# Optimization experiments

Hardware: AMD Instinct MI355X
Metric: run time of the kernel (lower is better)

Reference implementation:

```python
import jax, jax.numpy as jnp
import numpy as np

B, C, H, W = 4, 64, 64, 64
CI = C // 2  # inter_channels


def setup_inputs() -> dict:
    key = jax.random.key(0)
    k1, k2, k3, k4, k5 = jax.random.split(key, 5)
    x = jax.random.normal(k1, (B, C, H, W), dtype=jnp.float32)
    # 1x1 conv g: in C -> CI (weight [CI, C], bias [CI])
    Wg = jax.random.normal(k2, (CI, C), dtype=jnp.float32) * (1.0 / np.sqrt(C))
    bg = jax.random.normal(k3, (CI,), dtype=jnp.float32) * 0.01
    # 1x1 conv W_z: CI -> C
    Wz = jax.random.normal(k4, (C, CI), dtype=jnp.float32) * (1.0 / np.sqrt(CI))
    bz = jax.random.normal(k5, (C,), dtype=jnp.float32) * 0.01
    return {"x": x, "Wg": Wg, "bg": bg, "Wz": Wz, "bz": bz}


def reference(x, Wg, bg, Wz, bz):
    b, c, h, w = x.shape
    n = h * w
    xf = x.reshape(b, c, n)                       # [B,C,N]
    # g projection (1x1 conv) then flatten: [B,N,CI]
    g_x = jnp.einsum('bcn,oc->bno', xf, Wg) + bg  # [B,N,CI]
    # theta = phi = raw x flattened
    theta = xf.transpose(0, 2, 1)                 # [B,N,C]
    f = jnp.einsum('bnc,bcm->bnm', theta, xf)     # [B,N,N]
    f_div_C = jax.nn.softmax(f, axis=-1)
    y = jnp.einsum('bnm,bmo->bno', f_div_C, g_x)  # [B,N,CI]
    y = y.transpose(0, 2, 1).reshape(b, CI, h, w)  # [B,CI,H,W]
    # W_z projection (1x1 conv) + residual
    W_y = jnp.einsum('oi,bihw->bohw', Wz, y) + bz[None, :, None, None]
    return W_y + x
```

## Files before the change

kernel.cpp:

```cpp
#include <hip/hip_runtime.h>
#include <hip/hip_bf16.h>
#include <math.h>

#define B_  4
#define C_  64
#define N_  4096
#define CI_ 32

typedef __attribute__((ext_vector_type(8))) unsigned short u16x8;
typedef __attribute__((ext_vector_type(8))) __bf16        bf16x8;
typedef __attribute__((ext_vector_type(4))) float         f32x4;

__device__ __forceinline__ unsigned short f2bf(float f) {
    union { float f; unsigned int i; } v; v.f = f;
    unsigned int r = v.i + 0x7FFFu + ((v.i >> 16) & 1u);
    return (unsigned short)(r >> 16);
}

__global__ __launch_bounds__(256) void k_prep(
    const float* __restrict__ x, const float* __restrict__ Wg,
    const float* __restrict__ bg, unsigned short* __restrict__ xT,
    unsigned short* __restrict__ gx, float* __restrict__ diag)
{
    __shared__ __align__(16) float tile[64][68];
    __shared__ float part[4][64][33];
    const int t  = threadIdx.x;
    const int b  = blockIdx.x >> 6;
    const int n0 = (blockIdx.x & 63) * 64;

    #pragma unroll
    for (int pass = 0; pass < 4; ++pass) {
        int c   = (t >> 4) + pass * 16;
        int nl4 = (t & 15) * 4;
        float4 v = *(const float4*)(x + (size_t)(b * C_ + c) * N_ + n0 + nl4);
        *(float4*)&tile[c][nl4] = v;
    }
    __syncthreads();

    {
        const int n  = t >> 2;
        const int cc = (t & 3) * 16;
        u16x8 a, b2;
        #pragma unroll
        for (int j = 0; j < 8; ++j) a[j]  = f2bf(tile[cc + j][n]);
        #pragma unroll
        for (int j = 0; j < 8; ++j) b2[j] = f2bf(tile[cc + 8 + j][n]);
        unsigned short* dst = xT + (size_t)(b * N_ + n0 + n) * C_ + cc;
        *(u16x8*)dst       = a;
        *(u16x8*)(dst + 8) = b2;
    }
    {
        const int nl = t & 63, cq = t >> 6;
        float acc[CI_];
        #pragma unroll
        for (int o = 0; o < CI_; ++o) acc[o] = 0.f;
        float dd = 0.f;
        #pragma unroll 4
        for (int cl = 0; cl < 16; ++cl) {
            int c = cq * 16 + cl;
            float xv = tile[c][nl];
            dd += xv * xv;
            #pragma unroll
            for (int o = 0; o < CI_; ++o) acc[o] += Wg[o * C_ + c] * xv;
        }
        #pragma unroll
        for (int o = 0; o < CI_; ++o) part[cq][nl][o] = acc[o];
        part[cq][nl][32] = dd;
    }
    __syncthreads();
    {
        const int o = t >> 3, nr = (t & 7) * 8;
        u16x8 w;
        #pragma unroll
        for (int j = 0; j < 8; ++j) {
            int n = nr + j;
            float s = part[0][n][o] + part[1][n][o] + part[2][n][o] + part[3][n][o]
                    + bg[o];
            w[j] = f2bf(s);
        }
        *(u16x8*)(gx + (size_t)(b * CI_ + o) * N_ + n0 + nr) = w;
    }
    if (t < 64)
        diag[(size_t)b * N_ + n0 + t] =
            part[0][t][32] + part[1][t][32] + part[2][t][32] + part[3][t][32];
}

__device__ __forceinline__ f32x4 mfma16(bf16x8 a, bf16x8 b, f32x4 c) {
    return __builtin_amdgcn_mfma_f32_16x16x32_bf16(a, b, c, 0, 0, 0);
}

__global__ __launch_bounds__(256, 4) void k_flash(
    const unsigned short* __restrict__ xT, const unsigned short* __restrict__ gx,
    const float* __restrict__ diag,
    float* __restrict__ ypart, float* __restrict__ lpart)
{
    __shared__ __align__(16) char smem[24576];
    unsigned short* xk = (unsigned short*)smem;
    unsigned short* vt = (unsigned short*)(smem + 9216);
    unsigned short* Pl = (unsigned short*)(smem + 14336);

    const int tid  = threadIdx.x;
    const int wave = tid >> 6, lane = tid & 63;
    const int quad = lane >> 4, li = lane & 15;
    const int g = wave >> 1, qh = wave & 1;
    const int bi  = blockIdx.x;
    const int kq  = bi & 3;
    const int qtb = (bi >> 2) & 63;
    const int b   = bi >> 8;
    const int qw  = qtb * 64 + qh * 32;
    const int u   = tid & 127;

    float Kq[2];
    #pragma unroll
    for (int qt = 0; qt < 2; ++qt)
        Kq[qt] = diag[(size_t)b * N_ + qw + qt * 16 + li];

    bf16x8 Qf[2][2];
    #pragma unroll
    for (int qt = 0; qt < 2; ++qt)
        #pragma unroll
        for (int kc = 0; kc < 2; ++kc)
            Qf[qt][kc] = *(const bf16x8*)(xT + (size_t)(b * N_ + qw + qt * 16 + li) * C_
                                          + kc * 32 + quad * 8);

    f32x4 Yf[2][2];
    #pragma unroll
    for (int qt = 0; qt < 2; ++qt)
        #pragma unroll
        for (int ot = 0; ot < 2; ++ot)
            Yf[qt][ot] = (f32x4){0.f, 0.f, 0.f, 0.f};
    float lacc[2] = {0.f, 0.f};

    const int keybase = kq * 1024 + g * 512;

    for (int tl = 0; tl < 16; ++tl) {
        const int k0 = keybase + tl * 32;
        __syncthreads();
        #pragma unroll
        for (int j = 0; j < 2; ++j) {
            int cc2 = u * 2 + j;
            int key = cc2 >> 3, coff = (cc2 & 7) * 8;
            *(u16x8*)(xk + (g * 32 + key) * 72 + coff) =
                *(const u16x8*)(xT + (size_t)(b * N_ + k0 + key) * C_ + coff);
        }
        {
            int o = u >> 2, koff = (u & 3) * 8;
            *(u16x8*)(vt + (g * 32 + o) * 40 + koff) =
                *(const u16x8*)(gx + (size_t)(b * CI_ + o) * N_ + k0 + koff);
        }
        __syncthreads();

        bf16x8 A[2][2];
        #pragma unroll
        for (int kt = 0; kt < 2; ++kt)
            #pragma unroll
            for (int kc = 0; kc < 2; ++kc)
                A[kt][kc] = *(const bf16x8*)(xk + (g * 32 + kt * 16 + li) * 72
                                             + kc * 32 + quad * 8);
        f32x4 S[2][2];
        #pragma unroll
        for (int kt = 0; kt < 2; ++kt)
            #pragma unroll
            for (int qt = 0; qt < 2; ++qt) {
                f32x4 z = (f32x4){0.f, 0.f, 0.f, 0.f};
                z = mfma16(A[kt][0], Qf[qt][0], z);
                S[kt][qt] = mfma16(A[kt][1], Qf[qt][1], z);
            }

        #pragma unroll
        for (int qt = 0; qt < 2; ++qt) {
            float p[2][4];
            #pragma unroll
            for (int kt = 0; kt < 2; ++kt)
                #pragma unroll
                for (int r = 0; r < 4; ++r) {
                    p[kt][r] = __expf(S[kt][qt][r] - Kq[qt]);
                    lacc[qt] += p[kt][r];
                }
            #pragma unroll
            for (int kt = 0; kt < 2; ++kt) {
                uint2 wv;
                wv.x = (unsigned)f2bf(p[kt][0]) | ((unsigned)f2bf(p[kt][1]) << 16);
                wv.y = (unsigned)f2bf(p[kt][2]) | ((unsigned)f2bf(p[kt][3]) << 16);
                *(uint2*)(Pl + (wave * 32 + qt * 16 + li) * 40 + kt * 16 + quad * 4) = wv;
            }
        }

        bf16x8 Ap[2], Bv[2];
        #pragma unroll
        for (int qt = 0; qt < 2; ++qt)
            Ap[qt] = *(const bf16x8*)(Pl + (wave * 32 + qt * 16 + li) * 40 + quad * 8);
        #pragma unroll
        for (int ot = 0; ot < 2; ++ot)
            Bv[ot] = *(const bf16x8*)(vt + (g * 32 + ot * 16 + li) * 40 + quad * 8);
        #pragma unroll
        for (int qt = 0; qt < 2; ++qt)
            #pragma unroll
            for (int ot = 0; ot < 2; ++ot)
                Yf[qt][ot] = mfma16(Ap[qt], Bv[ot], Yf[qt][ot]);
    }

    #pragma unroll
    for (int qt = 0; qt < 2; ++qt) {
        lacc[qt] += __shfl_xor(lacc[qt], 16, 64);
        lacc[qt] += __shfl_xor(lacc[qt], 32, 64);
    }

    __syncthreads();
    float* ym = (float*)smem;

    #pragma unroll
    for (int qt = 0; qt < 2; ++qt) {
        #pragma unroll
        for (int ot = 0; ot < 2; ++ot)
            #pragma unroll
            for (int r = 0; r < 4; ++r)
                ym[(wave * 32 + qt * 16 + quad * 4 + r) * 34 + ot * 16 + li] = Yf[qt][ot][r];
        if (quad == 0)
            ym[(wave * 32 + qt * 16 + li) * 34 + 32] = lacc[qt];
    }
    __syncthreads();
    {
        const int q = tid >> 2, og = tid & 3;
        const int qh2 = q >> 5, ql = q & 31;
        const int w0 = qh2, w1 = 2 + qh2;
        const size_t pbase = (size_t)(b * 64 + qtb) * 4 + kq;
        float* yp = ypart + pbase * 2048 + q * 32;
        #pragma unroll
        for (int j = 0; j < 8; ++j) {
            int o = og * 8 + j;
            yp[o] = ym[(w0 * 32 + ql) * 34 + o] + ym[(w1 * 32 + ql) * 34 + o];
        }
        if (og == 0)
            lpart[pbase * 64 + q] = ym[(w0 * 32 + ql) * 34 + 32]
                                  + ym[(w1 * 32 + ql) * 34 + 32];
    }
}

__global__ __launch_bounds__(256) void k_merge(
    const float* __restrict__ ypart, const float* __restrict__ lpart,
    const float* __restrict__ x, const float* __restrict__ Wz,
    const float* __restrict__ bz, float* __restrict__ out)
{
    __shared__ float yfin[64][33];
    const int t   = threadIdx.x;
    const int b   = blockIdx.x >> 6;
    const int qtb = blockIdx.x & 63;
    const int q0  = qtb * 64;

    {
        const int q = t >> 2, og = t & 3;
        const size_t pb = (size_t)(b * 64 + qtb) * 4;
        float l = lpart[(pb + 0) * 64 + q] + lpart[(pb + 1) * 64 + q]
                + lpart[(pb + 2) * 64 + q] + lpart[(pb + 3) * 64 + q];
        float inv = 1.f / l;
        #pragma unroll
        for (int j = 0; j < 8; ++j) {
            int o = og * 8 + j;
            float acc = 0.f;
            #pragma unroll
            for (int kq = 0; kq < 4; ++kq)
                acc += ypart[(pb + kq) * 2048 + q * 32 + o];
            yfin[q][o] = acc * inv;
        }
    }
    __syncthreads();
    {
        const int q = t & 63, c0 = t >> 6;
        #pragma unroll
        for (int i = 0; i < 16; ++i) {
            int cout = c0 + i * 4;
            float acc = bz[cout];
            #pragma unroll
            for (int o = 0; o < CI_; ++o)
                acc += Wz[cout * CI_ + o] * yfin[q][o];
            size_t oidx = (size_t)(b * C_ + cout) * N_ + q0 + q;
            out[oidx] = acc + x[oidx];
        }
    }
}

extern "C" void kernel_launch(void* const* d_in, const int* in_sizes, int n_in,
                              void* d_out, int out_size, void* d_ws, size_t ws_size,
                              hipStream_t stream) {
    (void)in_sizes; (void)n_in; (void)out_size; (void)ws_size;
    const float* x  = (const float*)d_in[0];
    const float* Wg = (const float*)d_in[1];
    const float* bg = (const float*)d_in[2];
    const float* Wz = (const float*)d_in[3];
    const float* bz = (const float*)d_in[4];
    float* out = (float*)d_out;

    unsigned short* xT = (unsigned short*)d_ws;
    unsigned short* gx = (unsigned short*)((char*)d_ws + 2097152);
    float* diag  = (float*)((char*)d_ws + 3145728);
    float* ypart = (float*)((char*)d_ws + 3211264);
    float* lpart = (float*)((char*)d_ws + 11599872);

    hipLaunchKernelGGL(k_prep,  dim3(B_ * (N_ / 64)),    dim3(256), 0, stream, x, Wg, bg, xT, gx, diag);
    hipLaunchKernelGGL(k_flash, dim3(B_ * 64 * 4),       dim3(256), 0, stream, xT, gx, diag, ypart, lpart);
    hipLaunchKernelGGL(k_merge, dim3(B_ * 64),           dim3(256), 0, stream, ypart, lpart, x, Wz, bz, out);
}
```

Baseline: 115.0 us.

## Load K/V MFMA fragments directly from global memory, drop LDS staging and barriers

Removes the shared-memory staging of key and value tiles, and the two block-wide barriers per iteration, by loading MFMA operands straight from global memory (relying on L1/L2 caching). It also folds the softmax shift into the MFMA accumulator initialisation and uses native bf16 conversion instead of manual rounding. LDS use shrinks, which may raise occupancy. The cost is that each wave does its own uncoalesced global loads with no block-level reuse, and the P tile stays in LDS with no barrier between the per-wave write and read.

```diff
diff --git a/kernel.cpp b/kernel.cpp
--- a/kernel.cpp
+++ b/kernel.cpp
@@ -9,6 +9,7 @@
 
 typedef __attribute__((ext_vector_type(8))) unsigned short u16x8;
 typedef __attribute__((ext_vector_type(8))) __bf16        bf16x8;
+typedef __attribute__((ext_vector_type(4))) __bf16        bf16x4;
 typedef __attribute__((ext_vector_type(4))) float         f32x4;
 
 __device__ __forceinline__ unsigned short f2bf(float f) {
@@ -94,10 +95,8 @@
     const float* __restrict__ diag,
     float* __restrict__ ypart, float* __restrict__ lpart)
 {
-    __shared__ __align__(16) char smem[24576];
-    unsigned short* xk = (unsigned short*)smem;
-    unsigned short* vt = (unsigned short*)(smem + 9216);
-    unsigned short* Pl = (unsigned short*)(smem + 14336);
+    __shared__ __align__(16) char smem[17408];
+    unsigned short* Pl = (unsigned short*)smem;
 
     const int tid  = threadIdx.x;
     const int wave = tid >> 6, lane = tid & 63;
@@ -108,19 +107,21 @@
     const int qtb = (bi >> 2) & 63;
     const int b   = bi >> 8;
     const int qw  = qtb * 64 + qh * 32;
-    const int u   = tid & 127;
-
-    float Kq[2];
+
+    const unsigned short* xb = xT + (size_t)b * N_ * C_;
+    const unsigned short* gb = gx + (size_t)b * CI_ * N_;
+
+    float nKq[2];
     #pragma unroll
     for (int qt = 0; qt < 2; ++qt)
-        Kq[qt] = diag[(size_t)b * N_ + qw + qt * 16 + li];
+        nKq[qt] = -diag[(size_t)b * N_ + qw + qt * 16 + li];
 
     bf16x8 Qf[2][2];
     #pragma unroll
     for (int qt = 0; qt < 2; ++qt)
         #pragma unroll
         for (int kc = 0; kc < 2; ++kc)
-            Qf[qt][kc] = *(const bf16x8*)(xT + (size_t)(b * N_ + qw + qt * 16 + li) * C_
+            Qf[qt][kc] = *(const bf16x8*)(xb + (size_t)(qw + qt * 16 + li) * C_
                                           + kc * 32 + quad * 8);
 
     f32x4 Yf[2][2];
@@ -133,66 +134,54 @@
 
     const int keybase = kq * 1024 + g * 512;
 
+    const unsigned short* aBase  = xb + (size_t)(keybase + li) * C_ + quad * 8;
+    const unsigned short* bBase0 = gb + (size_t)(li) * N_      + keybase + quad * 8;
+    const unsigned short* bBase1 = gb + (size_t)(16 + li) * N_ + keybase + quad * 8;
+    unsigned short*       pW = Pl + (wave * 32 + li) * 40 + quad * 4;
+    const unsigned short* pR = Pl + (wave * 32 + li) * 40 + quad * 8;
+
     for (int tl = 0; tl < 16; ++tl) {
-        const int k0 = keybase + tl * 32;
-        __syncthreads();
-        #pragma unroll
-        for (int j = 0; j < 2; ++j) {
-            int cc2 = u * 2 + j;
-            int key = cc2 >> 3, coff = (cc2 & 7) * 8;
-            *(u16x8*)(xk + (g * 32 + key) * 72 + coff) =
-                *(const u16x8*)(xT + (size_t)(b * N_ + k0 + key) * C_ + coff);
-        }
-        {
-            int o = u >> 2, koff = (u & 3) * 8;
-            *(u16x8*)(vt + (g * 32 + o) * 40 + koff) =
-                *(const u16x8*)(gx + (size_t)(b * CI_ + o) * N_ + k0 + koff);
-        }
-        __syncthreads();
+        const int koff = tl * 32;
 
         bf16x8 A[2][2];
         #pragma unroll
         for (int kt = 0; kt < 2; ++kt)
             #pragma unroll
             for (int kc = 0; kc < 2; ++kc)
-                A[kt][kc] = *(const bf16x8*)(xk + (g * 32 + kt * 16 + li) * 72
-                                             + kc * 32 + quad * 8);
+                A[kt][kc] = *(const bf16x8*)(aBase + (size_t)(koff + kt * 16) * C_
+                                             + kc * 32);
+        bf16x8 Bv[2];
+        Bv[0] = *(const bf16x8*)(bBase0 + koff);
+        Bv[1] = *(const bf16x8*)(bBase1 + koff);
+
         f32x4 S[2][2];
         #pragma unroll
         for (int kt = 0; kt < 2; ++kt)
             #pragma unroll
             for (int qt = 0; qt < 2; ++qt) {
-                f32x4 z = (f32x4){0.f, 0.f, 0.f, 0.f};
+                f32x4 z = (f32x4){nKq[qt], nKq[qt], nKq[qt], nKq[qt]};
                 z = mfma16(A[kt][0], Qf[qt][0], z);
                 S[kt][qt] = mfma16(A[kt][1], Qf[qt][1], z);
             }
 
         #pragma unroll
-        for (int qt = 0; qt < 2; ++qt) {
-            float p[2][4];
-            #pragma unroll
-            for (int kt = 0; kt < 2; ++kt)
+        for (int qt = 0; qt < 2; ++qt)
+            #pragma unroll
+            for (int kt = 0; kt < 2; ++kt) {
+                bf16x4 pb;
                 #pragma unroll
                 for (int r = 0; r < 4; ++r) {
-                    p[kt][r] = __expf(S[kt][qt][r] - Kq[qt]);
-                    lacc[qt] += p[kt][r];
+                    float p = __expf(S[kt][qt][r]);
+                    lacc[qt] += p;
+                    pb[r] = (__bf16)p;
                 }
-            #pragma unroll
-            for (int kt = 0; kt < 2; ++kt) {
-                uint2 wv;
-                wv.x = (unsigned)f2bf(p[kt][0]) | ((unsigned)f2bf(p[kt][1]) << 16);
-                wv.y = (unsigned)f2bf(p[kt][2]) | ((unsigned)f2bf(p[kt][3]) << 16);
-                *(uint2*)(Pl + (wave * 32 + qt * 16 + li) * 40 + kt * 16 + quad * 4) = wv;
+                *(bf16x4*)(pW + qt * 640 + kt * 16) = pb;
             }
-        }
-
-        bf16x8 Ap[2], Bv[2];
+
+        bf16x8 Ap[2];
         #pragma unroll
         for (int qt = 0; qt < 2; ++qt)
-            Ap[qt] = *(const bf16x8*)(Pl + (wave * 32 + qt * 16 + li) * 40 + quad * 8);
-        #pragma unroll
-        for (int ot = 0; ot < 2; ++ot)
-            Bv[ot] = *(const bf16x8*)(vt + (g * 32 + ot * 16 + li) * 40 + quad * 8);
+            Ap[qt] = *(const bf16x8*)(pR + qt * 640);
         #pragma unroll
         for (int qt = 0; qt < 2; ++qt)
             #pragma unroll
```

After: 134.3 us. 1.17x slower.
